# Kernel optimization log

Hardware: AMD Instinct MI355X
Metric: run time of the kernel (lower is better)

## Reference

```python
import jax, jax.numpy as jnp
import numpy as np

EMB = 1024
HEADS = 16
HEAD_DIM = EMB // HEADS
DFF = 4 * EMB
EPS = 1e-5


def gelu_tanh(x):
    c = jnp.sqrt(jnp.asarray(2.0 / jnp.pi, dtype=x.dtype))
    return 0.5 * x * (1.0 + jnp.tanh(c * (x + 0.044715 * x ** 3)))


def layernorm(x, scale, shift):
    mean = jnp.mean(x, axis=-1, keepdims=True)
    var = jnp.mean((x - mean) ** 2, axis=-1, keepdims=True)
    return scale * ((x - mean) / jnp.sqrt(var + EPS)) + shift


def setup_inputs() -> dict:
    key = jax.random.key(0)
    ks = jax.random.split(key, 12)
    s = 0.02
    return {
        "x": jax.random.normal(ks[0], (2, 2048, EMB), dtype=jnp.float32),
        "Wq": jax.random.normal(ks[1], (EMB, EMB), dtype=jnp.float32) * s,
        "Wk": jax.random.normal(ks[2], (EMB, EMB), dtype=jnp.float32) * s,
        "Wv": jax.random.normal(ks[3], (EMB, EMB), dtype=jnp.float32) * s,
        "Wo": jax.random.normal(ks[4], (EMB, EMB), dtype=jnp.float32) * s,
        "bo": jnp.zeros((EMB,), dtype=jnp.float32),
        "W1": jax.random.normal(ks[5], (EMB, DFF), dtype=jnp.float32) * s,
        "b1": jnp.zeros((DFF,), dtype=jnp.float32),
        "W2": jax.random.normal(ks[6], (DFF, EMB), dtype=jnp.float32) * s,
        "b2": jnp.zeros((EMB,), dtype=jnp.float32),
        "g1": jnp.ones((EMB,), dtype=jnp.float32),
        "s1": jnp.zeros((EMB,), dtype=jnp.float32),
        "g2": jnp.ones((EMB,), dtype=jnp.float32),
        "s2": jnp.zeros((EMB,), dtype=jnp.float32),
    }


def reference(x, Wq, Wk, Wv, Wo, bo, W1, b1, W2, b2, g1, s1, g2, s2):
    B, S, E = x.shape
    # attention sub-block (pre-norm, residual)
    h = layernorm(x, g1, s1)
    Q = (h @ Wq).reshape(B, S, HEADS, HEAD_DIM)
    K = (h @ Wk).reshape(B, S, HEADS, HEAD_DIM)
    V = (h @ Wv).reshape(B, S, HEADS, HEAD_DIM)
    # scores: [B, H, S, S]
    scores = jnp.einsum("bqhd,bkhd->bhqk", Q, K)
    causal = jnp.tril(jnp.ones((S, S), dtype=bool))
    scores = jnp.where(causal, scores, -jnp.inf)
    attn = jax.nn.softmax(scores / np.sqrt(HEAD_DIM), axis=-1)
    ctx = jnp.einsum("bhqk,bkhd->bqhd", attn, V).reshape(B, S, E)
    x = x + (ctx @ Wo + bo)
    # FFN sub-block
    h = layernorm(x, g2, s2)
    h = gelu_tanh(h @ W1 + b1) @ W2 + b2
    return x + h
```

## Files before the change

### kernel.cpp

```cpp
#include <hip/hip_runtime.h>
#include <hip/hip_bf16.h>

typedef __attribute__((ext_vector_type(8))) short short8;
typedef __attribute__((ext_vector_type(4))) float f32x4;

#define EMB   1024
#define DFF   4096
#define S_LEN 2048
#define NB    2
#define MTOT  (NB * S_LEN)
#define HEADS 16
#define HDIM  64
#define QKN   2048

__device__ __forceinline__ float bf2f(unsigned short u) {
  return __uint_as_float(((unsigned int)u) << 16);
}
__device__ __forceinline__ unsigned short f2bf(float f) {
  unsigned int x = __float_as_uint(f);
  unsigned int r = (x + 0x7fffu + ((x >> 16) & 1u)) >> 16;
  return (unsigned short)r;
}
__device__ __forceinline__ unsigned int cvtpk(float a, float b) {
  unsigned int r;
  asm("v_cvt_pk_bf16_f32 %0, %1, %2" : "=v"(r) : "v"(a), "v"(b));
  return r;
}

__device__ __forceinline__ void gl_lds16(const unsigned short* g, unsigned short* l) {
  __builtin_amdgcn_global_load_lds(
      (const __attribute__((address_space(1))) unsigned int*)g,
      (__attribute__((address_space(3))) unsigned int*)l, 16, 0, 0);
}

__device__ __forceinline__ float gelu_tanh_f(float v) {
  float u = v + 0.044715f * v * v * v;
  float t = tanhf(0.7978845608028654f * u);
  return 0.5f * v * (1.0f + t);
}

__global__ __launch_bounds__(256) void fused_transpose(
    const float* __restrict__ Wq, const float* __restrict__ Wk,
    const float* __restrict__ Wv, const float* __restrict__ Wo,
    const float* __restrict__ W1, const float* __restrict__ W2,
    unsigned short* __restrict__ wtQ, unsigned short* __restrict__ wtK,
    unsigned short* __restrict__ wtV, unsigned short* __restrict__ wtO,
    unsigned short* __restrict__ wtW1, unsigned short* __restrict__ wtW2)
{
  __shared__ float t[64][33];
  const int bid = (int)blockIdx.x;
  const float* W; unsigned short* Wt; int K, N, local;
  if (bid < 2048) {
    const int sel = bid >> 9; local = bid & 511; K = 1024; N = 1024;
    W  = sel == 0 ? Wq  : sel == 1 ? Wk  : sel == 2 ? Wv  : Wo;
    Wt = sel == 0 ? wtQ : sel == 1 ? wtK : sel == 2 ? wtV : wtO;
  } else if (bid < 4096) {
    local = bid - 2048; K = 1024; N = 4096; W = W1; Wt = wtW1;
  } else {
    local = bid - 4096; K = 4096; N = 1024; W = W2; Wt = wtW2;
  }
  const int nbx = N >> 5;
  const int n0 = (local % nbx) * 32, k0 = (local / nbx) * 64;
  const int tx = threadIdx.x, ty = threadIdx.y;
#pragma unroll
  for (int i = 0; i < 8; ++i) {
    const int kr = i * 8 + ty;
    t[kr][tx] = W[(size_t)(k0 + kr) * N + n0 + tx];
  }
  __syncthreads();
#pragma unroll
  for (int i = 0; i < 4; ++i) {
    const int r = ty + i * 8;
    const unsigned int u = cvtpk(t[2 * tx][r], t[2 * tx + 1][r]);
    *(unsigned int*)(&Wt[(size_t)(n0 + r) * K + k0 + 2 * tx]) = u;
  }
}

__global__ __launch_bounds__(256) void ln_kernel(
    const float* __restrict__ X, const float* __restrict__ g,
    const float* __restrict__ sh, unsigned short* __restrict__ H)
{
  const int row = blockIdx.x, t = threadIdx.x;
  const float* xr = X + (size_t)row * EMB;
  float4 v = *(const float4*)(xr + t * 4);
  float s  = v.x + v.y + v.z + v.w;
  float ss = v.x * v.x + v.y * v.y + v.z * v.z + v.w * v.w;
#pragma unroll
  for (int off = 32; off > 0; off >>= 1) {
    s  += __shfl_xor(s, off);
    ss += __shfl_xor(ss, off);
  }
  __shared__ float rs[4], rss[4];
  const int wid = t >> 6;
  if ((t & 63) == 0) { rs[wid] = s; rss[wid] = ss; }
  __syncthreads();
  s  = rs[0] + rs[1] + rs[2] + rs[3];
  ss = rss[0] + rss[1] + rss[2] + rss[3];
  const float mean = s * (1.f / EMB);
  const float var  = ss * (1.f / EMB) - mean * mean;
  const float rstd = rsqrtf(var + 1e-5f);
  float4 gv = *(const float4*)(g + t * 4);
  float4 sv = *(const float4*)(sh + t * 4);
  ushort4 o;
  o.x = f2bf((v.x - mean) * rstd * gv.x + sv.x);
  o.y = f2bf((v.y - mean) * rstd * gv.y + sv.y);
  o.z = f2bf((v.z - mean) * rstd * gv.z + sv.z);
  o.w = f2bf((v.w - mean) * rstd * gv.w + sv.w);
  *(ushort4*)(H + (size_t)row * EMB + t * 4) = o;
}

__global__ __launch_bounds__(512, 2) void gemm256(
    const unsigned short* __restrict__ A, const unsigned short* __restrict__ Bt,
    const float* __restrict__ bias, unsigned short* __restrict__ outb)
{
  __shared__ unsigned short As[2][256 * 64];
  __shared__ unsigned short Bs[2][256 * 64];

  const int tid = threadIdx.x;
  const int lane = tid & 63, wid = tid >> 6;
  const int bid = (int)blockIdx.x;
  const int swz = (bid & 7) * 32 + (bid >> 3);
  const int by = swz >> 4, bx = swz & 15;
  const int m0 = by * 256, n0 = bx * 256;
  const int wr = wid >> 2, wc = wid & 3;
  const int l16 = lane & 15, kg = lane >> 4;

  const int sr  = lane >> 3;
  const int scs = ((lane & 7) ^ (lane >> 3)) * 8;
  const int rx  = l16 & 7;

  const unsigned short* Abase = A + (size_t)m0 * 1024;
  const unsigned short* Bbase = Bt + (size_t)n0 * 1024;

  f32x4 acc[8][4];
#pragma unroll
  for (int i = 0; i < 8; ++i)
#pragma unroll
    for (int j = 0; j < 4; ++j) acc[i][j] = (f32x4){0.f, 0.f, 0.f, 0.f};

#define STG256(buf, t)                                                         \
  do {                                                                         \
    const int k0_ = (t) * 64;                                                  \
    _Pragma("unroll")                                                          \
    for (int i_ = 0; i_ < 4; ++i_) {                                           \
      const int ca_ = wid * 4 + i_;                                            \
      gl_lds16(Abase + (size_t)(ca_ * 8 + sr) * 1024 + k0_ + scs,              \
               &As[buf][ca_ * 512]);                                           \
      gl_lds16(Bbase + (size_t)(ca_ * 8 + sr) * 1024 + k0_ + scs,              \
               &Bs[buf][ca_ * 512]);                                           \
    }                                                                          \
  } while (0)

  STG256(0, 0);
  asm volatile("s_waitcnt vmcnt(0)" ::: "memory");
  __builtin_amdgcn_s_barrier();

  const int nt = 1024 / 64;
  for (int t = 0; t < nt; ++t) {
    const int b = t & 1;
    if (t + 1 < nt) STG256(b ^ 1, t + 1);
#pragma unroll
    for (int kk = 0; kk < 2; ++kk) {
      short8 af[8];
#pragma unroll
      for (int i = 0; i < 8; ++i) {
        const int row = wr * 128 + i * 16 + l16;
        af[i] = *(const short8*)(&As[b][row * 64 + ((kg + kk * 4) ^ rx) * 8]);
      }
      __builtin_amdgcn_s_setprio(1);
#pragma unroll
      for (int j = 0; j < 4; ++j) {
        const int row = wc * 64 + j * 16 + l16;
        short8 bf = *(const short8*)(&Bs[b][row * 64 + ((kg + kk * 4) ^ rx) * 8]);
#pragma unroll
        for (int i = 0; i < 8; ++i)
          acc[i][j] = __builtin_amdgcn_mfma_f32_16x16x32_bf16(af[i], bf, acc[i][j], 0, 0, 0);
      }
      __builtin_amdgcn_s_setprio(0);
    }
    asm volatile("s_waitcnt lgkmcnt(0)" ::: "memory");
    asm volatile("s_waitcnt vmcnt(0)" ::: "memory");
    __builtin_amdgcn_s_barrier();
  }
#undef STG256

#pragma unroll
  for (int i = 0; i < 8; ++i) {
#pragma unroll
    for (int j = 0; j < 4; ++j) {
      const int c = n0 + wc * 64 + j * 16 + l16;
      const float bc = bias[c];
#pragma unroll
      for (int r = 0; r < 4; ++r) {
        const int row = m0 + wr * 128 + i * 16 + kg * 4 + r;
        outb[(size_t)row * 4096 + c] = f2bf(gelu_tanh_f(acc[i][j][r] + bc));
      }
    }
  }
}

template <int MODE, int BN, int BKT, int NBUF>
__global__ __launch_bounds__(256, 2) void gemm_gl(
    const unsigned short* __restrict__ A, const unsigned short* __restrict__ Bt,
    int M, int N, int Kloop, int Kld, int nbx,
    const float* __restrict__ bias, const float* __restrict__ resf,
    float* __restrict__ outf, unsigned short* __restrict__ outb,
    unsigned short* __restrict__ vt)
{
  constexpr int NFRAG = BN / 32;
  constexpr int KK    = BKT / 32;
  constexpr int ACH   = 128 * BKT / 512;
  constexpr int BCH   = BN  * BKT / 512;
  __shared__ unsigned short As[NBUF][128 * BKT];
  __shared__ unsigned short Bs[NBUF][BN * BKT];

  const int tid = threadIdx.x;
  const int lane = tid & 63, wid = tid >> 6;
  const int nwg = (int)gridDim.x;
  const int cpx = nwg >> 3;
  const int bid = (int)blockIdx.x;
  const int swz = (bid & 7) * cpx + (bid >> 3);
  const int by = swz / nbx;
  const int bx = swz - by * nbx;
  const int m0 = by * 128, n0 = bx * BN;
  const int wr = wid >> 1, wc = wid & 1;
  const int l16 = lane & 15, kg = lane >> 4;

  int sr, scs;
  if constexpr (BKT == 32) {
    sr  = lane >> 2;
    scs = ((lane & 3) ^ ((lane >> 3) & 3)) * 8;
  } else {
    sr  = lane >> 3;
    scs = ((lane & 7) ^ (lane >> 3)) * 8;
  }
  const int rx = (BKT == 32) ? ((l16 >> 1) & 3) : (l16 & 7);

  const unsigned short* Abase = A + (size_t)m0 * Kld;
  const unsigned short* Bbase = Bt + (size_t)n0 * Kld;

  f32x4 acc[4][NFRAG];
#pragma unroll
  for (int i = 0; i < 4; ++i)
#pragma unroll
    for (int j = 0; j < NFRAG; ++j) acc[i][j] = (f32x4){0.f, 0.f, 0.f, 0.f};

  const int nt = Kloop / BKT;
  constexpr int RPC = (BKT == 32) ? 16 : 8;

#define STAGE(buf, t)                                                          \
  do {                                                                         \
    const int k0_ = (t) * BKT;                                                 \
    _Pragma("unroll")                                                          \
    for (int i_ = 0; i_ < ACH / 4; ++i_) {                                     \
      const int chunk_ = wid * (ACH / 4) + i_;                                 \
      gl_lds16(Abase + (size_t)(chunk_ * RPC + sr) * Kld + k0_ + scs,          \
               &As[buf][0] + chunk_ * 512);                                    \
    }                                                                          \
    _Pragma("unroll")                                                          \
    for (int i_ = 0; i_ < BCH / 4; ++i_) {                                     \
      const int chunk_ = wid * (BCH / 4) + i_;                                 \
      gl_lds16(Bbase + (size_t)(chunk_ * RPC + sr) * Kld + k0_ + scs,          \
               &Bs[buf][0] + chunk_ * 512);                                    \
    }                                                                          \
  } while (0)

#define VM_WAIT()                                                              \
  do {                                                                         \
    constexpr int W_ = ((ACH + BCH) / 4) * (NBUF - 1);                         \
    if constexpr (W_ == 3)      asm volatile("s_waitcnt vmcnt(3)" ::: "memory"); \
    else if constexpr (W_ == 4) asm volatile("s_waitcnt vmcnt(4)" ::: "memory"); \
    else if constexpr (W_ == 6) asm volatile("s_waitcnt vmcnt(6)" ::: "memory"); \
    else if constexpr (W_ == 8) asm volatile("s_waitcnt vmcnt(8)" ::: "memory"); \
    else                        asm volatile("s_waitcnt vmcnt(12)" ::: "memory"); \
  } while (0)

  STAGE(0, 0);
  STAGE(1, 1);
  if constexpr (NBUF == 3) STAGE(2, 2);
  VM_WAIT();
  __builtin_amdgcn_s_barrier();

  int b = 0;
  for (int t = 0; t < nt; ++t) {
    short8 af[4][KK], bfr[NFRAG][KK];
#pragma unroll
    for (int i = 0; i < 4; ++i)
#pragma unroll
      for (int kk = 0; kk < KK; ++kk)
        af[i][kk] = *(const short8*)(
            &As[b][(wr * 64 + i * 16 + l16) * BKT + ((kg + kk * 4) ^ rx) * 8]);
#pragma unroll
    for (int j = 0; j < NFRAG; ++j)
#pragma unroll
      for (int kk = 0; kk < KK; ++kk)
        bfr[j][kk] = *(const short8*)(
            &Bs[b][(wc * (BN / 2) + j * 16 + l16) * BKT + ((kg + kk * 4) ^ rx) * 8]);
#pragma unroll
    for (int kk = 0; kk < KK; ++kk)
#pragma unroll
      for (int i = 0; i < 4; ++i)
#pragma unroll
        for (int j = 0; j < NFRAG; ++j)
          acc[i][j] = __builtin_amdgcn_mfma_f32_16x16x32_bf16(af[i][kk], bfr[j][kk], acc[i][j], 0, 0, 0);
    asm volatile("s_waitcnt lgkmcnt(0)" ::: "memory");
    __builtin_amdgcn_s_barrier();
    if (t + NBUF < nt) {
      STAGE(b, t + NBUF);
      VM_WAIT();
    } else {
      asm volatile("s_waitcnt vmcnt(0)" ::: "memory");
    }
    __builtin_amdgcn_s_barrier();
    if constexpr (NBUF == 2) b ^= 1;
    else                     b = (b == 2) ? 0 : b + 1;
  }
#undef STAGE
#undef VM_WAIT

#pragma unroll
  for (int i = 0; i < 4; ++i) {
#pragma unroll
    for (int j = 0; j < NFRAG; ++j) {
      const int c = n0 + wc * (BN / 2) + j * 16 + l16;
      if constexpr (MODE == 0) {
        if (c >= 2048) {
          const int row0 = m0 + wr * 64 + i * 16 + kg * 4;
          const int dcol = c - 2048;
          ushort4 w4;
          w4.x = f2bf(acc[i][j][0]); w4.y = f2bf(acc[i][j][1]);
          w4.z = f2bf(acc[i][j][2]); w4.w = f2bf(acc[i][j][3]);
          *(ushort4*)(&vt[((size_t)((row0 >> 11) * 16 + (dcol >> 6)) * 64 +
                           (dcol & 63)) * 2048 + (row0 & 2047)]) = w4;
        } else {
          const float sc = (c < 1024) ? 0.18033688011112042f : 1.0f;
#pragma unroll
          for (int r = 0; r < 4; ++r) {
            const int row = m0 + wr * 64 + i * 16 + kg * 4 + r;
            outb[(size_t)row * QKN + c] = f2bf(acc[i][j][r] * sc);
          }
        }
      } else {
#pragma unroll
        for (int r = 0; r < 4; ++r) {
          const int row = m0 + wr * 64 + i * 16 + kg * 4 + r;
          const size_t idx = (size_t)row * N + c;
          float v = acc[i][j][r];
          if constexpr (MODE == 1) {
            outf[idx] = v + bias[c] + resf[idx];
          } else if constexpr (MODE == 2) {
            outb[idx] = f2bf(gelu_tanh_f(v + bias[c]));
          } else {
            outf[idx] = v + bias[c] + resf[idx];
          }
        }
      }
    }
  }
}

__global__ __launch_bounds__(256) void attn_mfma(
    const unsigned short* __restrict__ qkv, const unsigned short* __restrict__ Vt,
    unsigned short* __restrict__ ctx)
{
  __shared__ unsigned short Ks[128][64];
  __shared__ unsigned short Vs[64][128];
  __shared__ unsigned short Ps[4][2][16][128];

  const int tid  = threadIdx.x;
  const int lane = tid & 63, wv = tid >> 6;
  const int l16  = lane & 15, kg = lane >> 4;
  const int bid  = (int)blockIdx.x;
  const int swz  = (bid & 7) * 64 + (bid >> 3);
  const int pair = swz & 15;
  const int bh   = swz >> 4;
  const int b    = bh >> 4, h = bh & 15;
  const int qtg0 = pair;
  const int qtg1 = 31 - pair;

  const size_t qbase  = ((size_t)b * S_LEN) * QKN + h * HDIM;
  const size_t kbase  = qbase + 1024;
  const size_t vtbase = ((size_t)bh * HDIM) * S_LEN;
  const size_t cbase  = ((size_t)b * S_LEN) * EMB + h * HDIM;

  short8 qf[2][2];
#pragma unroll
  for (int g = 0; g < 2; ++g) {
    const int qt = g ? qtg1 : qtg0;
    const unsigned short* qrow =
        qkv + qbase + (size_t)(qt * 64 + wv * 16 + l16) * QKN;
    qf[g][0] = *(const short8*)(qrow + kg * 8);
    qf[g][1] = *(const short8*)(qrow + 32 + kg * 8);
  }

  f32x4 o[2][4];
#pragma unroll
  for (int g = 0; g < 2; ++g)
#pragma unroll
    for (int dt = 0; dt < 4; ++dt) o[g][dt] = (f32x4){0.f, 0.f, 0.f, 0.f};
  float m[2] = {-1e30f, -1e30f}, l[2] = {0.f, 0.f};

  const int kr2 = tid >> 1, kh = tid & 1;
  const int ksx = kr2 & 7;
  const int vr = tid >> 2, vc = tid & 3;
  const int vsx = vr & 7;
  const int rx = l16 & 7;

  const int nkt = (qtg1 + 2) >> 1;

  const unsigned short* ksrc = qkv + kbase + (size_t)kr2 * QKN + kh * 32;
  const unsigned short* vsrc = Vt + vtbase + (size_t)vr * S_LEN + vc * 32;
  short8 kv0 = *(const short8*)(ksrc);
  short8 kv1 = *(const short8*)(ksrc + 8);
  short8 kv2 = *(const short8*)(ksrc + 16);
  short8 kv3 = *(const short8*)(ksrc + 24);
  short8 vv0 = *(const short8*)(vsrc);
  short8 vv1 = *(const short8*)(vsrc + 8);
  short8 vv2 = *(const short8*)(vsrc + 16);
  short8 vv3 = *(const short8*)(vsrc + 24);

  for (int kt = 0; kt < nkt; ++kt) {
    __syncthreads();
    *(short8*)(&Ks[kr2][((kh * 4 + 0) ^ ksx) * 8]) = kv0;
    *(short8*)(&Ks[kr2][((kh * 4 + 1) ^ ksx) * 8]) = kv1;
    *(short8*)(&Ks[kr2][((kh * 4 + 2) ^ ksx) * 8]) = kv2;
    *(short8*)(&Ks[kr2][((kh * 4 + 3) ^ ksx) * 8]) = kv3;
    *(short8*)(&Vs[vr][((vc * 4 + 0) ^ vsx) * 8]) = vv0;
    *(short8*)(&Vs[vr][((vc * 4 + 1) ^ vsx) * 8]) = vv1;
    *(short8*)(&Vs[vr][((vc * 4 + 2) ^ vsx) * 8]) = vv2;
    *(short8*)(&Vs[vr][((vc * 4 + 3) ^ vsx) * 8]) = vv3;
    __syncthreads();

    if (kt + 1 < nkt) {
      const unsigned short* kn =
          qkv + kbase + (size_t)((kt + 1) * 128 + kr2) * QKN + kh * 32;
      const unsigned short* vn =
          Vt + vtbase + (size_t)vr * S_LEN + (kt + 1) * 128 + vc * 32;
      kv0 = *(const short8*)(kn);
      kv1 = *(const short8*)(kn + 8);
      kv2 = *(const short8*)(kn + 16);
      kv3 = *(const short8*)(kn + 24);
      vv0 = *(const short8*)(vn);
      vv1 = *(const short8*)(vn + 8);
      vv2 = *(const short8*)(vn + 16);
      vv3 = *(const short8*)(vn + 24);
    }

    const bool act0 = (2 * kt <= qtg0);

    float fac[2] = {1.f, 1.f};
    bool resc[2] = {false, false};
#pragma unroll
    for (int g = 0; g < 2; ++g) {
      if (g == 0 && !act0) continue;
      const int qt = g ? qtg1 : qtg0;

      f32x4 sa[8];
      __builtin_amdgcn_s_setprio(1);
#pragma unroll
      for (int j = 0; j < 8; ++j) {
        short8 kf0 = *(const short8*)(&Ks[j * 16 + l16][(kg ^ rx) * 8]);
        short8 kf1 = *(const short8*)(&Ks[j * 16 + l16][((kg + 4) ^ rx) * 8]);
        sa[j] = (f32x4){0.f, 0.f, 0.f, 0.f};
        sa[j] = __builtin_amdgcn_mfma_f32_16x16x32_bf16(kf0, qf[g][0], sa[j], 0, 0, 0);
        sa[j] = __builtin_amdgcn_mfma_f32_16x16x32_bf16(kf1, qf[g][1], sa[j], 0, 0, 0);
      }
      __builtin_amdgcn_s_setprio(0);

      const int qloc = qt * 64 + wv * 16 + l16;
      if (kt * 128 + 127 > qt * 64 + wv * 16) {
#pragma unroll
        for (int j = 0; j < 8; ++j)
#pragma unroll
          for (int r = 0; r < 4; ++r)
            if (kt * 128 + j * 16 + kg * 4 + r > qloc) sa[j][r] = -1e30f;
      }

      float mx = fmaxf(fmaxf(sa[0][0], sa[0][1]), fmaxf(sa[0][2], sa[0][3]));
#pragma unroll
      for (int j = 1; j < 8; ++j) {
        float mj = fmaxf(fmaxf(sa[j][0], sa[j][1]), fmaxf(sa[j][2], sa[j][3]));
        mx = fmaxf(mx, mj);
      }
      mx = fmaxf(mx, __shfl_xor(mx, 16));
      mx = fmaxf(mx, __shfl_xor(mx, 32));
      if (!__all(mx - m[g] <= 8.0f)) {
        const float mn = fmaxf(m[g], mx);
        fac[g] = exp2f(m[g] - mn);
        m[g] = mn;
        resc[g] = true;
      }
      const float mcur = m[g];
      float ps = 0.f;
#pragma unroll
      for (int j = 0; j < 8; ++j) {
        float p0 = exp2f(sa[j][0] - mcur);
        float p1 = exp2f(sa[j][1] - mcur);
        float p2 = exp2f(sa[j][2] - mcur);
        float p3 = exp2f(sa[j][3] - mcur);
        sa[j][0] = p0; sa[j][1] = p1; sa[j][2] = p2; sa[j][3] = p3;
        ps += (p0 + p1) + (p2 + p3);
      }
      ps += __shfl_xor(ps, 16);
      ps += __shfl_xor(ps, 32);
      l[g] = l[g] * fac[g] + ps;

#pragma unroll
      for (int j = 0; j < 8; ++j) {
        uint2 pw;
        pw.x = cvtpk(sa[j][0], sa[j][1]);
        pw.y = cvtpk(sa[j][2], sa[j][3]);
        *(uint2*)(&Ps[wv][g][l16][((2 * j + (kg >> 1)) ^ rx) * 8 + (kg & 1) * 4]) = pw;
      }
    }

#pragma unroll
    for (int g = 0; g < 2; ++g) {
      if (resc[g]) {
#pragma unroll
        for (int dt = 0; dt < 4; ++dt)
#pragma unroll
          for (int r = 0; r < 4; ++r) o[g][dt][r] *= fac[g];
      }
    }

    short8 pf[2][4];
#pragma unroll
    for (int g = 0; g < 2; ++g) {
      if (g == 0 && !act0) continue;
#pragma unroll
      for (int s = 0; s < 4; ++s)
        pf[g][s] = *(const short8*)(&Ps[wv][g][l16][((4 * s + kg) ^ rx) * 8]);
    }
    __builtin_amdgcn_s_setprio(1);
#pragma unroll
    for (int dt = 0; dt < 4; ++dt) {
#pragma unroll
      for (int s = 0; s < 4; ++s) {
        short8 vf = *(const short8*)(&Vs[dt * 16 + l16][((4 * s + kg) ^ rx) * 8]);
#pragma unroll
        for (int g = 0; g < 2; ++g) {
          if (g == 0 && !act0) continue;
          o[g][dt] = __builtin_amdgcn_mfma_f32_16x16x32_bf16(vf, pf[g][s], o[g][dt], 0, 0, 0);
        }
      }
    }
    __builtin_amdgcn_s_setprio(0);
  }

#pragma unroll
  for (int g = 0; g < 2; ++g) {
    const int qt = g ? qtg1 : qtg0;
    const float inv = 1.0f / l[g];
    const int qrow = qt * 64 + wv * 16 + l16;
#pragma unroll
    for (int dt = 0; dt < 4; ++dt) {
      uint2 cw;
      cw.x = cvtpk(o[g][dt][0] * inv, o[g][dt][1] * inv);
      cw.y = cvtpk(o[g][dt][2] * inv, o[g][dt][3] * inv);
      *(uint2*)(&ctx[cbase + (size_t)qrow * EMB + dt * 16 + kg * 4]) = cw;
    }
  }
}

extern "C" void kernel_launch(void* const* d_in, const int* in_sizes, int n_in,
                              void* d_out, int out_size, void* d_ws, size_t ws_size,
                              hipStream_t stream)
{
  const float* x  = (const float*)d_in[0];
  const float* Wq = (const float*)d_in[1];
  const float* Wk = (const float*)d_in[2];
  const float* Wv = (const float*)d_in[3];
  const float* Wo = (const float*)d_in[4];
  const float* bo = (const float*)d_in[5];
  const float* W1 = (const float*)d_in[6];
  const float* b1 = (const float*)d_in[7];
  const float* W2 = (const float*)d_in[8];
  const float* b2 = (const float*)d_in[9];
  const float* g1 = (const float*)d_in[10];
  const float* s1 = (const float*)d_in[11];
  const float* g2 = (const float*)d_in[12];
  const float* s2 = (const float*)d_in[13];

  float* out = (float*)d_out;
  char* ws = (char*)d_ws;
  const size_t MB = 1024 * 1024;
  unsigned short* wtQ  = (unsigned short*)(ws + 0 * MB);
  unsigned short* wtK  = (unsigned short*)(ws + 2 * MB);
  unsigned short* wtV  = (unsigned short*)(ws + 4 * MB);
  unsigned short* wtO  = (unsigned short*)(ws + 6 * MB);
  unsigned short* wtW1 = (unsigned short*)(ws + 8 * MB);
  unsigned short* wtW2 = (unsigned short*)(ws + 16 * MB);
  unsigned short* h    = (unsigned short*)(ws + 24 * MB);
  unsigned short* qkv  = (unsigned short*)(ws + 32 * MB);
  unsigned short* Vt   = (unsigned short*)(ws + 56 * MB);
  unsigned short* ctxb = h;
  unsigned short* h2   = h;
  unsigned short* gbuf = qkv;

  fused_transpose<<<dim3(6144), dim3(32, 8), 0, stream>>>(
      Wq, Wk, Wv, Wo, W1, W2, wtQ, wtK, wtV, wtO, wtW1, wtW2);

  ln_kernel<<<MTOT, 256, 0, stream>>>(x, g1, s1, h);

  gemm_gl<0, 128, 32, 2><<<dim3(24 * 32), 256, 0, stream>>>(
      h, wtQ, MTOT, 3072, 1024, 1024, 24, nullptr, nullptr, nullptr, qkv, Vt);

  attn_mfma<<<dim3(512), 256, 0, stream>>>(qkv, Vt, ctxb);

  gemm_gl<1, 64, 64, 2><<<dim3(16 * 32), 256, 0, stream>>>(
      ctxb, wtO, MTOT, 1024, 1024, 1024, 16, bo, x, out, nullptr, nullptr);

  ln_kernel<<<MTOT, 256, 0, stream>>>(out, g2, s2, h2);

  gemm256<<<dim3(256), 512, 0, stream>>>(h2, wtW1, b1, gbuf);

  gemm_gl<3, 64, 64, 2><<<dim3(16 * 32), 256, 0, stream>>>(
      gbuf, wtW2, MTOT, 1024, DFF, DFF, 16, b2, out, out, nullptr, nullptr);
}
```

Baseline: 237.6 us.

## Restructure W1 GEMM main loop into four-phase ping-pong pipeline with split staging

Rewrites the 256x256 FFN-up GEMM main loop into four phases per k-tile. Each phase loads a slice of A fragments, issues half-tile global-to-LDS loads, and runs MFMAs, with barriers between phases. B fragments are held in registers for the whole tile, so the B buffer can be refilled two tiles ahead while A is refilled one tile ahead. The aim is to interleave memory traffic with compute and avoid the single full vmcnt(0) drain per iteration. In exchange it adds more barriers and a more delicate buffer-reuse order.

```diff
diff --git a/kernel.cpp b/kernel.cpp
--- a/kernel.cpp
+++ b/kernel.cpp
@@ -109,7 +109,7 @@
   *(ushort4*)(H + (size_t)row * EMB + t * 4) = o;
 }
 
-__global__ __launch_bounds__(512, 2) void gemm256(
+__global__ __launch_bounds__(512, 2) void gemm8p(
     const unsigned short* __restrict__ A, const unsigned short* __restrict__ Bt,
     const float* __restrict__ bias, unsigned short* __restrict__ outb)
 {
@@ -129,8 +129,8 @@
   const int scs = ((lane & 7) ^ (lane >> 3)) * 8;
   const int rx  = l16 & 7;
 
-  const unsigned short* Abase = A + (size_t)m0 * 1024;
-  const unsigned short* Bbase = Bt + (size_t)n0 * 1024;
+  const unsigned short* Ab = A + (size_t)m0 * 1024;
+  const unsigned short* Bb = Bt + (size_t)n0 * 1024;
 
   f32x4 acc[8][4];
 #pragma unroll
@@ -138,51 +138,70 @@
 #pragma unroll
     for (int j = 0; j < 4; ++j) acc[i][j] = (f32x4){0.f, 0.f, 0.f, 0.f};
 
-#define STG256(buf, t)                                                         \
+#define STGH(ldsdst, gb, grow0, kt_)                                           \
   do {                                                                         \
-    const int k0_ = (t) * 64;                                                  \
     _Pragma("unroll")                                                          \
-    for (int i_ = 0; i_ < 4; ++i_) {                                           \
-      const int ca_ = wid * 4 + i_;                                            \
-      gl_lds16(Abase + (size_t)(ca_ * 8 + sr) * 1024 + k0_ + scs,              \
-               &As[buf][ca_ * 512]);                                           \
-      gl_lds16(Bbase + (size_t)(ca_ * 8 + sr) * 1024 + k0_ + scs,              \
-               &Bs[buf][ca_ * 512]);                                           \
+    for (int i_ = 0; i_ < 2; ++i_) {                                           \
+      const int c_ = wid * 2 + i_;                                             \
+      gl_lds16((gb) + (size_t)((grow0) + c_ * 8 + sr) * 1024 + (kt_) * 64 + scs, \
+               (ldsdst) + c_ * 512);                                           \
     }                                                                          \
   } while (0)
 
-  STG256(0, 0);
-  asm volatile("s_waitcnt vmcnt(0)" ::: "memory");
+#define PHASE(mp, STAGE_STMT, TAIL_STMT)                                       \
+  do {                                                                         \
+    short8 af[2][2];                                                           \
+    _Pragma("unroll")                                                          \
+    for (int i = 0; i < 2; ++i)                                                \
+      _Pragma("unroll")                                                        \
+      for (int kk = 0; kk < 2; ++kk)                                           \
+        af[i][kk] = *(const short8*)(                                          \
+            &As[b][(wr * 128 + ((mp) * 2 + i) * 16 + l16) * 64 +               \
+                   ((kg + kk * 4) ^ rx) * 8]);                                 \
+    STAGE_STMT;                                                                \
+    __builtin_amdgcn_s_barrier();                                              \
+    asm volatile("s_waitcnt lgkmcnt(0)" ::: "memory");                         \
+    __builtin_amdgcn_s_setprio(1);                                             \
+    _Pragma("unroll")                                                          \
+    for (int kk = 0; kk < 2; ++kk)                                             \
+      _Pragma("unroll")                                                        \
+      for (int j = 0; j < 4; ++j)                                              \
+        _Pragma("unroll")                                                      \
+        for (int i = 0; i < 2; ++i)                                            \
+          acc[(mp) * 2 + i][j] = __builtin_amdgcn_mfma_f32_16x16x32_bf16(      \
+              af[i][kk], bf[j][kk], acc[(mp) * 2 + i][j], 0, 0, 0);            \
+    __builtin_amdgcn_s_setprio(0);                                             \
+    TAIL_STMT;                                                                 \
+    __builtin_amdgcn_s_barrier();                                              \
+  } while (0)
+
+  STGH(&As[0][0], Ab, 0, 0);   STGH(&As[0][128 * 64], Ab, 128, 0);
+  STGH(&Bs[0][0], Bb, 0, 0);   STGH(&Bs[0][128 * 64], Bb, 128, 0);
+  STGH(&As[1][0], Ab, 0, 1);   STGH(&As[1][128 * 64], Ab, 128, 1);
+  STGH(&Bs[1][0], Bb, 0, 1);   STGH(&Bs[1][128 * 64], Bb, 128, 1);
+  asm volatile("s_waitcnt vmcnt(8)" ::: "memory");
   __builtin_amdgcn_s_barrier();
 
-  const int nt = 1024 / 64;
+  const int nt = 16;
   for (int t = 0; t < nt; ++t) {
     const int b = t & 1;
-    if (t + 1 < nt) STG256(b ^ 1, t + 1);
-#pragma unroll
-    for (int kk = 0; kk < 2; ++kk) {
-      short8 af[8];
-#pragma unroll
-      for (int i = 0; i < 8; ++i) {
-        const int row = wr * 128 + i * 16 + l16;
-        af[i] = *(const short8*)(&As[b][row * 64 + ((kg + kk * 4) ^ rx) * 8]);
-      }
-      __builtin_amdgcn_s_setprio(1);
-#pragma unroll
-      for (int j = 0; j < 4; ++j) {
-        const int row = wc * 64 + j * 16 + l16;
-        short8 bf = *(const short8*)(&Bs[b][row * 64 + ((kg + kk * 4) ^ rx) * 8]);
-#pragma unroll
-        for (int i = 0; i < 8; ++i)
-          acc[i][j] = __builtin_amdgcn_mfma_f32_16x16x32_bf16(af[i], bf, acc[i][j], 0, 0, 0);
-      }
-      __builtin_amdgcn_s_setprio(0);
-    }
-    asm volatile("s_waitcnt lgkmcnt(0)" ::: "memory");
-    asm volatile("s_waitcnt vmcnt(0)" ::: "memory");
-    __builtin_amdgcn_s_barrier();
-  }
-#undef STG256
+    short8 bf[4][2];
+#pragma unroll
+    for (int j = 0; j < 4; ++j)
+#pragma unroll
+      for (int kk = 0; kk < 2; ++kk)
+        bf[j][kk] = *(const short8*)(
+            &Bs[b][(wc * 64 + j * 16 + l16) * 64 + ((kg + kk * 4) ^ rx) * 8]);
+
+    PHASE(0, if (t >= 1 && t + 1 < nt) STGH(&As[b ^ 1][0], Ab, 0, t + 1), );
+    PHASE(1, if (t >= 1 && t + 1 < nt) STGH(&As[b ^ 1][128 * 64], Ab, 128, t + 1), );
+    PHASE(2, if (t + 2 < nt) STGH(&Bs[b][0], Bb, 0, t + 2), );
+    PHASE(3, if (t + 2 < nt) STGH(&Bs[b][128 * 64], Bb, 128, t + 2),
+          if (t + 2 < nt) { asm volatile("s_waitcnt vmcnt(4)" ::: "memory"); }
+          else            { asm volatile("s_waitcnt vmcnt(0)" ::: "memory"); });
+  }
+#undef PHASE
+#undef STGH
 
 #pragma unroll
   for (int i = 0; i < 8; ++i) {
@@ -613,7 +632,7 @@
 
   ln_kernel<<<MTOT, 256, 0, stream>>>(out, g2, s2, h2);
 
-  gemm256<<<dim3(256), 512, 0, stream>>>(h2, wtW1, b1, gbuf);
+  gemm8p<<<dim3(256), 512, 0, stream>>>(h2, wtW1, b1, gbuf);
 
   gemm_gl<3, 64, 64, 2><<<dim3(16 * 32), 256, 0, stream>>>(
       gbuf, wtW2, MTOT, 1024, DFF, DFF, 16, b2, out, out, nullptr, nullptr);
```

New measurement: 235.3 us. About the same (-1.0%).
